# Kernel optimization log

Measured on AMD Instinct MI355X. Metric: run time of the kernel, lower is better.

## Reference

```python
import jax, jax.numpy as jnp
import numpy as np

B, CIN, COUT, H, W = 4, 256, 256, 64, 64
K, G = 3, 4
PAD = (K - 1) // 2


def setup_inputs() -> dict:
    key = jax.random.key(0)
    k0, k1, k2, k3 = jax.random.split(key, 4)
    x = jax.random.normal(k0, (B, CIN, H, W), jnp.float32)
    y = jax.random.normal(k1, (B, 2, H, W), jnp.float32)
    # conv_offset: 1x1 conv, no bias, init std=0.1 (normal_init)
    w_offset = jax.random.normal(k2, (G * 2 * K * K, 2, 1, 1), jnp.float32) * 0.1
    # DeformConv2d weight, no bias, init std=0.01
    w_deform = jax.random.normal(k3, (COUT, CIN, K, K), jnp.float32) * 0.01
    return {"x": x, "y": y, "w_offset": w_offset, "w_deform": w_deform}


def _deform_conv(x, offset, weight):
    """DCN v1: stride 1, dilation 1, zero padding PAD, deform_groups=G, groups=1."""
    KK = K * K
    # mmcv offset layout: [B, G*2*KK, H, W] -> per group, per kernel pos, (dy, dx)
    off = offset.reshape(B, G, KK, 2, H, W)
    dy, dx = off[:, :, :, 0], off[:, :, :, 1]            # [B,G,KK,H,W]
    ii, jj = jnp.meshgrid(jnp.arange(K), jnp.arange(K), indexing="ij")
    ky = ii.reshape(KK).astype(x.dtype)                  # kernel row offsets
    kx = jj.reshape(KK).astype(x.dtype)                  # kernel col offsets
    base_y = jnp.arange(H, dtype=x.dtype)[None, :, None] - PAD + ky[:, None, None]  # [KK,H,1]
    base_x = jnp.arange(W, dtype=x.dtype)[None, None, :] - PAD + kx[:, None, None]  # [KK,1,W]
    yc = dy + base_y                                     # [B,G,KK,H,W]
    xc = dx + base_x

    Cg = CIN // G
    xg = x.reshape(B, G, Cg, H, W)

    def sample(xg1, yc1, xc1):
        # xg1 [Cg,H,W]; yc1/xc1 [KK,H,W] -> bilinear sample with zero padding
        y0 = jnp.floor(yc1)
        x0 = jnp.floor(xc1)
        wy = yc1 - y0
        wx = xc1 - x0
        y0i = y0.astype(jnp.int32)
        x0i = x0.astype(jnp.int32)

        def gather(yi, xi):
            valid = (yi >= 0) & (yi < H) & (xi >= 0) & (xi < W)
            v = xg1[:, jnp.clip(yi, 0, H - 1), jnp.clip(xi, 0, W - 1)]  # [Cg,KK,H,W]
            return v * valid[None].astype(xg1.dtype)

        v00 = gather(y0i, x0i)
        v01 = gather(y0i, x0i + 1)
        v10 = gather(y0i + 1, x0i)
        v11 = gather(y0i + 1, x0i + 1)
        return (v00 * (1 - wy) * (1 - wx) + v01 * (1 - wy) * wx
                + v10 * wy * (1 - wx) + v11 * wy * wx)

    sampled = jax.vmap(jax.vmap(sample))(xg, yc, xc)     # [B,G,Cg,KK,H,W]
    sampled = sampled.reshape(B, CIN, KK, H, W)
    wflat = weight.reshape(COUT, CIN, KK)
    return jnp.einsum("bckhw,ock->bohw", sampled, wflat)  # [B,COUT,H,W]


def reference(x, y, w_offset, w_deform):
    # offset = conv_offset(y.detach()), a 1x1 conv without bias
    y_det = jax.lax.stop_gradient(y)
    offset = jnp.einsum("bihw,oi->bohw", y_det, w_offset[:, :, 0, 0])
    out = _deform_conv(x, offset, w_deform)
    return jax.nn.relu(out)
```

## Files before the change

### kernel.cpp

```cpp
#include <hip/hip_runtime.h>
#include <cstddef>

#define B_    4
#define CIN_  256
#define COUT_ 256
#define H_    64
#define W_    64
#define KK_   9
#define G_    4
#define NP    18
#define PW    80
#define PH    80
#define PADO  8

typedef short bf16x8 __attribute__((ext_vector_type(8)));
typedef float f32x4  __attribute__((ext_vector_type(4)));
typedef __attribute__((address_space(1))) const unsigned int* gptr_t;
typedef __attribute__((address_space(3))) unsigned int*       lptr_t;

__device__ __forceinline__ unsigned short f2bf(float v) {
    unsigned int u = __float_as_uint(v);
    u += 0x7fffu + ((u >> 16) & 1u);
    return (unsigned short)(u >> 16);
}
__device__ __forceinline__ float f_lo(unsigned int u) { return __uint_as_float(u << 16); }
__device__ __forceinline__ float f_hi(unsigned int u) { return __uint_as_float(u & 0xffff0000u); }

__global__ __launch_bounds__(256) void prep_kernel(const float* __restrict__ x,
                                                   unsigned short* __restrict__ xTp,
                                                   const float* __restrict__ w,
                                                   unsigned short* __restrict__ wb) {
    const int tid = threadIdx.x;
    if (blockIdx.x < 512) {
        __shared__ unsigned short s[128][66];
        const int bh    = blockIdx.x >> 1;
        const int chalf = blockIdx.x & 1;
        const int b     = bh >> 6, h = bh & 63;
        const size_t src_base = ((size_t)b * CIN_ + chalf * 128) * (H_ * W_) + h * W_;
        #pragma unroll 4
        for (int k = 0; k < 32; ++k) {
            int i = k * 256 + tid;
            int c = i >> 6, ww = i & 63;
            s[c][ww] = f2bf(x[src_base + (size_t)c * (H_ * W_) + ww]);
        }
        __syncthreads();
        const size_t dst_row = ((size_t)b * PH + (h + PADO)) * PW;
        #pragma unroll 4
        for (int k = 0; k < 20; ++k) {
            int j  = k * 256 + tid;
            int c2 = (j & 63) * 2, wp = j >> 6;
            unsigned int v = 0;
            if (wp >= PADO && wp < PADO + W_) {
                int ww = wp - PADO;
                v = (unsigned int)s[c2][ww] | ((unsigned int)s[c2 + 1][ww] << 16);
            }
            *(unsigned int*)(xTp + (dst_row + wp) * 256 + chalf * 128 + c2) = v;
        }
    } else if (blockIdx.x < 576) {
        const int bidx = blockIdx.x - 512;
        const int b = bidx >> 4, rr = bidx & 15;
        const int yp = (rr < PADO) ? rr : (PH - 16 + rr);
        unsigned short* dst = xTp + ((size_t)b * PH + yp) * PW * 256;
        #pragma unroll
        for (int k = 0; k < 10; ++k) {
            *(uint4*)(dst + (size_t)(k * 256 + tid) * 8) = make_uint4(0, 0, 0, 0);
        }
    } else {
        int idx = (blockIdx.x - 576) * 256 + tid;
        int e   = idx & 7;
        int pos = (idx >> 3) & 7;
        int o   = (idx >> 6) & 255;
        int t   = idx >> 14;
        int g   = t / 9, kk = t - g * 9;
        int j   = pos ^ (o & 7);
        int c   = g * 64 + j * 8 + e;
        wb[idx] = f2bf(w[(o * CIN_ + c) * KK_ + kk]);
    }
}

__global__ __launch_bounds__(512, 2) void dcn_kernel(
    const unsigned short* __restrict__ xTp, const float* __restrict__ y,
    const float* __restrict__ w_off, const unsigned short* __restrict__ wb,
    float* __restrict__ out)
{
    __shared__ unsigned short s_W[2][2][16384];
    __shared__ unsigned short s_S[2][2][4096];

    const int tid = threadIdx.x;
    const int bid = blockIdx.x;
    const int xcd = bid & 7;
    const int b   = xcd >> 1;
    const int h   = (xcd & 1) * 32 + (bid >> 3);

    const int sp = tid >> 3;
    const int c8 = tid & 7;

    const float yv0 = y[((b * 2 + 0) * H_ + h) * W_ + sp];
    const float yv1 = y[((b * 2 + 1) * H_ + h) * W_ + sp];
    const float spf = (float)(sp - 1 + PADO);
    const float hpf = (float)(h  - 1 + PADO);

    const int lane = tid & 63, wave = tid >> 6;
    const int pg  = wave & 1, oh = wave >> 1;
    const int l15 = lane & 15, kq = lane >> 4, sw = l15 & 7;

    f32x4 acc[8];
    #pragma unroll
    for (int i = 0; i < 8; ++i) acc[i] = (f32x4){0.f, 0.f, 0.f, 0.f};

    const unsigned short* xb = xTp + (size_t)b * (PH * PW * 256) + c8 * 8;

    float wgt[2][4];
    uint4 gA[2], gB[2], gC[2], gD[2];

#define ISSUE_ONE(t, P) do {                                                   \
    const int t_ = (t);                                                        \
    const int g_ = t_ / 9, kk_ = t_ - g_ * 9;                                  \
    const float4 co = *(const float4*)(w_off + t_ * 4);                        \
    const float dy = fmaf(yv0, co.x, yv1 * co.y);                              \
    const float dx = fmaf(yv0, co.z, yv1 * co.w);                              \
    const float yc = hpf + (float)(kk_ / 3) + dy;                              \
    const float xc = spf + (float)(kk_ % 3) + dx;                              \
    const float yf = floorf(yc), xf = floorf(xc);                              \
    const float wy = yc - yf, wx = xc - xf;                                    \
    const int   yi = (int)yf, xi = (int)xf;           \
    const float omy = 1.f - wy, omx = 1.f - wx;                                \
    wgt[P][0] = omy * omx; wgt[P][1] = omy * wx;                               \
    wgt[P][2] = wy * omx;  wgt[P][3] = wy * wx;                                \
    const unsigned short* p0 = xb + (yi * PW + xi) * 256 + g_ * 64;            \
    const unsigned short* p1 = p0 + PW * 256;                                  \
    gA[P] = *(const uint4*)(p0);        gB[P] = *(const uint4*)(p0 + 256);     \
    gC[P] = *(const uint4*)(p1);        gD[P] = *(const uint4*)(p1 + 256);     \
} while (0)

#define STAGE_W2(t, buf) do {                                                  \
    const unsigned short* src = wb + (size_t)(t) * 32768;                      \
    _Pragma("unroll")                                                          \
    for (int j = 0; j < 8; ++j) {                                              \
        const int off = (j * 512 + tid) * 8;                                   \
        __builtin_amdgcn_global_load_lds((gptr_t)(src + off),                  \
                                         (lptr_t)(&s_W[buf][0][0] + off),      \
                                         16, 0, 0);                            \
    }                                                                          \
} while (0)

#define WRITE_ONE(P, SB) do {                                                  \
    const unsigned int av[4] = {gA[P].x, gA[P].y, gA[P].z, gA[P].w};           \
    const unsigned int bv[4] = {gB[P].x, gB[P].y, gB[P].z, gB[P].w};           \
    const unsigned int cv[4] = {gC[P].x, gC[P].y, gC[P].z, gC[P].w};           \
    const unsigned int dv[4] = {gD[P].x, gD[P].y, gD[P].z, gD[P].w};           \
    unsigned int res[4];                                                       \
    _Pragma("unroll")                                                          \
    for (int q = 0; q < 4; ++q) {                                              \
        float rl = wgt[P][0] * f_lo(av[q]);                                    \
        rl = fmaf(wgt[P][1], f_lo(bv[q]), rl);                                 \
        rl = fmaf(wgt[P][2], f_lo(cv[q]), rl);                                 \
        rl = fmaf(wgt[P][3], f_lo(dv[q]), rl);                                 \
        float rh = wgt[P][0] * f_hi(av[q]);                                    \
        rh = fmaf(wgt[P][1], f_hi(bv[q]), rh);                                 \
        rh = fmaf(wgt[P][2], f_hi(cv[q]), rh);                                 \
        rh = fmaf(wgt[P][3], f_hi(dv[q]), rh);                                 \
        res[q] = __builtin_amdgcn_perm(__float_as_uint(rh),                    \
                                       __float_as_uint(rl), 0x07060302u);      \
    }                                                                          \
    *(uint4*)(&s_S[SB][P][0] + sp * 64 + ((c8 ^ (sp & 7)) * 8)) =              \
        make_uint4(res[0], res[1], res[2], res[3]);                            \
} while (0)

#define MFMA_TAP(WB, HF, SB) do {                                              \
    bf16x8 bf[2][2], af[2][4];                                                 \
    _Pragma("unroll")                                                          \
    for (int kh = 0; kh < 2; ++kh) {                                           \
        const int pos = ((kh * 4 + kq) ^ sw) * 8;                              \
        _Pragma("unroll")                                                      \
        for (int nt = 0; nt < 2; ++nt)                                         \
            bf[kh][nt] = *(const bf16x8*)(&s_S[SB][HF][0] +                    \
                              (pg * 32 + nt * 16 + l15) * 64 + pos);           \
        _Pragma("unroll")                                                      \
        for (int mt = 0; mt < 4; ++mt)                                         \
            af[kh][mt] = *(const bf16x8*)(&s_W[WB][HF][0] +                    \
                              (oh * 64 + mt * 16 + l15) * 64 + pos);           \
    }                                                                          \
    __builtin_amdgcn_s_setprio(1);                                             \
    _Pragma("unroll")                                                          \
    for (int kh = 0; kh < 2; ++kh)                                             \
        _Pragma("unroll")                                                      \
        for (int nt = 0; nt < 2; ++nt)                                         \
            _Pragma("unroll")                                                  \
            for (int mt = 0; mt < 4; ++mt)                                     \
                acc[nt * 4 + mt] = __builtin_amdgcn_mfma_f32_16x16x32_bf16(    \
                    af[kh][mt], bf[kh][nt], acc[nt * 4 + mt], 0, 0, 0);        \
    __builtin_amdgcn_s_setprio(0);                                             \
} while (0)

#define STEP(s_, P, DO_PF) do {                                                \
    if (DO_PF) { ISSUE_ONE(2 * (s_) + 2, 0); ISSUE_ONE(2 * (s_) + 3, 1); }     \
    __builtin_amdgcn_sched_barrier(0);                                         \
    if (DO_PF) STAGE_W2((s_) + 1, P ^ 1);                                      \
    __builtin_amdgcn_sched_barrier(0);                                         \
    MFMA_TAP(P, 0, P);                                                         \
    MFMA_TAP(P, 1, P);                                                         \
    __builtin_amdgcn_sched_barrier(0);                                         \
    if (DO_PF) { WRITE_ONE(0, P ^ 1); WRITE_ONE(1, P ^ 1); }                   \
    __builtin_amdgcn_sched_barrier(0);                                         \
    asm volatile("s_waitcnt vmcnt(0) lgkmcnt(0)" ::: "memory");                \
    __builtin_amdgcn_sched_barrier(0);                                         \
    __builtin_amdgcn_s_barrier();                                              \
    __builtin_amdgcn_sched_barrier(0);                                         \
} while (0)

    ISSUE_ONE(0, 0);
    ISSUE_ONE(1, 1);
    __builtin_amdgcn_sched_barrier(0);
    STAGE_W2(0, 0);
    __builtin_amdgcn_sched_barrier(0);
    WRITE_ONE(0, 0);
    WRITE_ONE(1, 0);
    __builtin_amdgcn_sched_barrier(0);
    asm volatile("s_waitcnt vmcnt(0) lgkmcnt(0)" ::: "memory");
    __builtin_amdgcn_sched_barrier(0);
    __builtin_amdgcn_s_barrier();
    __builtin_amdgcn_sched_barrier(0);

    for (int sb = 0; sb < 16; sb += 2) {
        STEP(sb + 0, 0, 1);
        STEP(sb + 1, 1, 1);
    }
    STEP(16, 0, 1);
    MFMA_TAP(1, 0, 1);
    MFMA_TAP(1, 1, 1);

    #pragma unroll
    for (int nt = 0; nt < 2; ++nt) {
        const int px = pg * 32 + nt * 16 + l15;
        #pragma unroll
        for (int mt = 0; mt < 4; ++mt) {
            const int obase = oh * 64 + mt * 16 + kq * 4;
            #pragma unroll
            for (int rr = 0; rr < 4; ++rr) {
                out[(((size_t)b * COUT_ + obase + rr) * H_ + h) * W_ + px] =
                    fmaxf(acc[nt * 4 + mt][rr], 0.f);
            }
        }
    }
#undef ISSUE_ONE
#undef STAGE_W2
#undef WRITE_ONE
#undef MFMA_TAP
#undef STEP
}

extern "C" void kernel_launch(void* const* d_in, const int* in_sizes, int n_in,
                              void* d_out, int out_size, void* d_ws, size_t ws_size,
                              hipStream_t stream) {
    const float* x     = (const float*)d_in[0];
    const float* y     = (const float*)d_in[1];
    const float* w_off = (const float*)d_in[2];
    const float* w_def = (const float*)d_in[3];
    float* out = (float*)d_out;

    unsigned short* xTp = (unsigned short*)d_ws;
    unsigned short* wb  = (unsigned short*)d_ws + (size_t)B_ * PH * PW * 256;

    prep_kernel<<<2880, 256, 0, stream>>>(x, xTp, w_def, wb);
    dcn_kernel<<<256, 512, 0, stream>>>(xTp, y, w_off, wb, out);
}
```

Before: 121.1 us.

## Warp-specialize DCN kernel into producer and MFMA consumer waves

Splits the 512-thread block so waves 4-7 only gather and bilinearly sample input and stage weight tiles into LDS, while waves 0-3 only run MFMAs, each covering 64 output channels and all 64 pixels. Weight staging moves to a triple buffer with one tap per stage, and sample staging to a double buffer, with partial vmcnt waits so global loads stay in flight across barriers. The intent is to overlap gather latency with matrix math instead of serializing them in every wave. In exchange each producer thread does twice the gather work, consumers hold 16 accumulators, and every tap now needs a block barrier.

```diff
diff --git a/kernel.cpp b/kernel.cpp
--- a/kernel.cpp
+++ b/kernel.cpp
@@ -8,7 +8,6 @@
 #define W_    64
 #define KK_   9
 #define G_    4
-#define NP    18
 #define PW    80
 #define PH    80
 #define PADO  8
@@ -83,37 +82,38 @@
     const float* __restrict__ w_off, const unsigned short* __restrict__ wb,
     float* __restrict__ out)
 {
-    __shared__ unsigned short s_W[2][2][16384];
-    __shared__ unsigned short s_S[2][2][4096];
+    __shared__ unsigned short s_W[3][16384];
+    __shared__ unsigned short s_S[2][4096];
 
     const int tid = threadIdx.x;
     const int bid = blockIdx.x;
     const int xcd = bid & 7;
     const int b   = xcd >> 1;
     const int h   = (xcd & 1) * 32 + (bid >> 3);
-
-    const int sp = tid >> 3;
-    const int c8 = tid & 7;
-
-    const float yv0 = y[((b * 2 + 0) * H_ + h) * W_ + sp];
-    const float yv1 = y[((b * 2 + 1) * H_ + h) * W_ + sp];
-    const float spf = (float)(sp - 1 + PADO);
-    const float hpf = (float)(h  - 1 + PADO);
-
     const int lane = tid & 63, wave = tid >> 6;
-    const int pg  = wave & 1, oh = wave >> 1;
-    const int l15 = lane & 15, kq = lane >> 4, sw = l15 & 7;
-
-    f32x4 acc[8];
-    #pragma unroll
-    for (int i = 0; i < 8; ++i) acc[i] = (f32x4){0.f, 0.f, 0.f, 0.f};
-
-    const unsigned short* xb = xTp + (size_t)b * (PH * PW * 256) + c8 * 8;
-
-    float wgt[2][4];
-    uint4 gA[2], gB[2], gC[2], gD[2];
-
-#define ISSUE_ONE(t, P) do {                                                   \
+
+#define BAR() do {                                                             \
+    __builtin_amdgcn_sched_barrier(0);                                         \
+    __builtin_amdgcn_s_barrier();                                              \
+    __builtin_amdgcn_sched_barrier(0);                                         \
+} while (0)
+
+    if (wave >= 4) {
+        const int ptid = tid - 256;
+        const int sp = ptid >> 2;
+        const int cq = (ptid & 3) * 2;
+
+        const float yv0 = y[((b * 2 + 0) * H_ + h) * W_ + sp];
+        const float yv1 = y[((b * 2 + 1) * H_ + h) * W_ + sp];
+        const float spf = (float)(sp - 1 + PADO);
+        const float hpf = (float)(h  - 1 + PADO);
+
+        const unsigned short* xb = xTp + (size_t)b * (PH * PW * 256) + cq * 8;
+
+        float wgt[2][4];
+        uint4 gA[2][2], gB[2][2], gC[2][2], gD[2][2];
+
+#define ISSUE_G(t, P) do {                                                     \
     const int t_ = (t);                                                        \
     const int g_ = t_ / 9, kk_ = t_ - g_ * 9;                                  \
     const float4 co = *(const float4*)(w_off + t_ * 4);                        \
@@ -129,27 +129,28 @@
     wgt[P][2] = wy * omx;  wgt[P][3] = wy * wx;                                \
     const unsigned short* p0 = xb + (yi * PW + xi) * 256 + g_ * 64;            \
     const unsigned short* p1 = p0 + PW * 256;                                  \
-    gA[P] = *(const uint4*)(p0);        gB[P] = *(const uint4*)(p0 + 256);     \
-    gC[P] = *(const uint4*)(p1);        gD[P] = *(const uint4*)(p1 + 256);     \
-} while (0)
-
-#define STAGE_W2(t, buf) do {                                                  \
-    const unsigned short* src = wb + (size_t)(t) * 32768;                      \
+    gA[P][0] = *(const uint4*)(p0);         gA[P][1] = *(const uint4*)(p0+8);  \
+    gB[P][0] = *(const uint4*)(p0 + 256);   gB[P][1] = *(const uint4*)(p0+264);\
+    gC[P][0] = *(const uint4*)(p1);         gC[P][1] = *(const uint4*)(p1+8);  \
+    gD[P][0] = *(const uint4*)(p1 + 256);   gD[P][1] = *(const uint4*)(p1+264);\
+} while (0)
+
+#define STAGE_W(t, buf) do {                                                   \
+    const unsigned short* src = wb + (size_t)(t) * 16384;                      \
     _Pragma("unroll")                                                          \
     for (int j = 0; j < 8; ++j) {                                              \
-        const int off = (j * 512 + tid) * 8;                                   \
+        const int off = (j * 256 + ptid) * 8;                                  \
         __builtin_amdgcn_global_load_lds((gptr_t)(src + off),                  \
-                                         (lptr_t)(&s_W[buf][0][0] + off),      \
+                                         (lptr_t)(&s_W[buf][0] + off),         \
                                          16, 0, 0);                            \
     }                                                                          \
 } while (0)
 
-#define WRITE_ONE(P, SB) do {                                                  \
-    const unsigned int av[4] = {gA[P].x, gA[P].y, gA[P].z, gA[P].w};           \
-    const unsigned int bv[4] = {gB[P].x, gB[P].y, gB[P].z, gB[P].w};           \
-    const unsigned int cv[4] = {gC[P].x, gC[P].y, gC[P].z, gC[P].w};           \
-    const unsigned int dv[4] = {gD[P].x, gD[P].y, gD[P].z, gD[P].w};           \
-    unsigned int res[4];                                                       \
+#define BIL1(Aq, Bq, Cq, Dq, P, res) do {                                      \
+    const unsigned int av[4] = {Aq.x, Aq.y, Aq.z, Aq.w};                       \
+    const unsigned int bv[4] = {Bq.x, Bq.y, Bq.z, Bq.w};                       \
+    const unsigned int cv[4] = {Cq.x, Cq.y, Cq.z, Cq.w};                       \
+    const unsigned int dv[4] = {Dq.x, Dq.y, Dq.z, Dq.w};                       \
     _Pragma("unroll")                                                          \
     for (int q = 0; q < 4; ++q) {                                              \
         float rl = wgt[P][0] * f_lo(av[q]);                                    \
@@ -163,91 +164,143 @@
         res[q] = __builtin_amdgcn_perm(__float_as_uint(rh),                    \
                                        __float_as_uint(rl), 0x07060302u);      \
     }                                                                          \
-    *(uint4*)(&s_S[SB][P][0] + sp * 64 + ((c8 ^ (sp & 7)) * 8)) =              \
-        make_uint4(res[0], res[1], res[2], res[3]);                            \
-} while (0)
-
-#define MFMA_TAP(WB, HF, SB) do {                                              \
-    bf16x8 bf[2][2], af[2][4];                                                 \
-    _Pragma("unroll")                                                          \
-    for (int kh = 0; kh < 2; ++kh) {                                           \
-        const int pos = ((kh * 4 + kq) ^ sw) * 8;                              \
-        _Pragma("unroll")                                                      \
-        for (int nt = 0; nt < 2; ++nt)                                         \
-            bf[kh][nt] = *(const bf16x8*)(&s_S[SB][HF][0] +                    \
-                              (pg * 32 + nt * 16 + l15) * 64 + pos);           \
+} while (0)
+
+#define BILIN2(P, SB) do {                                                     \
+    unsigned int r0[4], r1[4];                                                 \
+    BIL1(gA[P][0], gB[P][0], gC[P][0], gD[P][0], P, r0);                       \
+    BIL1(gA[P][1], gB[P][1], gC[P][1], gD[P][1], P, r1);                       \
+    *(uint4*)(&s_S[SB][0] + sp * 64 + (((cq + 0) ^ (sp & 7)) * 8)) =           \
+        make_uint4(r0[0], r0[1], r0[2], r0[3]);                                \
+    *(uint4*)(&s_S[SB][0] + sp * 64 + (((cq + 1) ^ (sp & 7)) * 8)) =           \
+        make_uint4(r1[0], r1[1], r1[2], r1[3]);                                \
+} while (0)
+
+#define PTAP(t, GSN, DBUF, GSO, SBUF) do {                                     \
+    ISSUE_G((t) + 2, GSN);                                                     \
+    __builtin_amdgcn_sched_barrier(0);                                         \
+    STAGE_W((t) + 2, DBUF);                                                    \
+    __builtin_amdgcn_sched_barrier(0);                                         \
+    asm volatile("s_waitcnt vmcnt(24)" ::: "memory");                          \
+    __builtin_amdgcn_sched_barrier(0);                                         \
+    BILIN2(GSO, SBUF);                                                         \
+    __builtin_amdgcn_sched_barrier(0);                                         \
+    asm volatile("s_waitcnt vmcnt(16) lgkmcnt(0)" ::: "memory");               \
+    BAR();                                                                     \
+} while (0)
+
+        ISSUE_G(0, 0);
+        __builtin_amdgcn_sched_barrier(0);
+        STAGE_W(0, 0);
+        __builtin_amdgcn_sched_barrier(0);
+        ISSUE_G(1, 1);
+        __builtin_amdgcn_sched_barrier(0);
+        STAGE_W(1, 1);
+        __builtin_amdgcn_sched_barrier(0);
+        asm volatile("s_waitcnt vmcnt(24)" ::: "memory");
+        __builtin_amdgcn_sched_barrier(0);
+        BILIN2(0, 0);
+        __builtin_amdgcn_sched_barrier(0);
+        asm volatile("s_waitcnt vmcnt(16) lgkmcnt(0)" ::: "memory");
+        BAR();
+
+        for (int tb = 0; tb < 30; tb += 6) {
+            PTAP(tb + 0, 0, 2, 1, 1);
+            PTAP(tb + 1, 1, 0, 0, 0);
+            PTAP(tb + 2, 0, 1, 1, 1);
+            PTAP(tb + 3, 1, 2, 0, 0);
+            PTAP(tb + 4, 0, 0, 1, 1);
+            PTAP(tb + 5, 1, 1, 0, 0);
+        }
+        PTAP(30, 0, 2, 1, 1);
+        PTAP(31, 1, 0, 0, 0);
+        PTAP(32, 0, 1, 1, 1);
+        PTAP(33, 1, 2, 0, 0);
+        asm volatile("s_waitcnt vmcnt(8)" ::: "memory");
+        __builtin_amdgcn_sched_barrier(0);
+        BILIN2(1, 1);
+        __builtin_amdgcn_sched_barrier(0);
+        asm volatile("s_waitcnt vmcnt(0) lgkmcnt(0)" ::: "memory");
+        BAR();
+        BAR();
+#undef ISSUE_G
+#undef STAGE_W
+#undef BIL1
+#undef BILIN2
+#undef PTAP
+    } else {
+        const int c   = wave;
+        const int l15 = lane & 15, kq = lane >> 4, swz = l15 & 7;
+        const int p0  = (kq ^ swz) * 8;
+        const int p1  = ((4 + kq) ^ swz) * 8;
+
+        const unsigned short* wbs[3] = {
+            &s_W[0][0] + (c * 64 + l15) * 64,
+            &s_W[1][0] + (c * 64 + l15) * 64,
+            &s_W[2][0] + (c * 64 + l15) * 64 };
+        const unsigned short* sbs[2] = {
+            &s_S[0][0] + l15 * 64,
+            &s_S[1][0] + l15 * 64 };
+
+        f32x4 acc[16];
+        #pragma unroll
+        for (int i = 0; i < 16; ++i) acc[i] = (f32x4){0.f, 0.f, 0.f, 0.f};
+
+#define CTAP(WB, SB) do {                                                      \
+    bf16x8 af0[4], af1[4], bf0[4], bf1[4];                                     \
+    _Pragma("unroll")                                                          \
+    for (int mt = 0; mt < 4; ++mt) {                                           \
+        af0[mt] = *(const bf16x8*)(wbs[WB] + mt * 1024 + p0);                  \
+        af1[mt] = *(const bf16x8*)(wbs[WB] + mt * 1024 + p1);                  \
+    }                                                                          \
+    _Pragma("unroll")                                                          \
+    for (int nt = 0; nt < 4; ++nt) {                                           \
+        bf0[nt] = *(const bf16x8*)(sbs[SB] + nt * 1024 + p0);                  \
+        bf1[nt] = *(const bf16x8*)(sbs[SB] + nt * 1024 + p1);                  \
+    }                                                                          \
+    __builtin_amdgcn_s_setprio(1);                                             \
+    _Pragma("unroll")                                                          \
+    for (int nt = 0; nt < 4; ++nt)                                             \
         _Pragma("unroll")                                                      \
         for (int mt = 0; mt < 4; ++mt)                                         \
-            af[kh][mt] = *(const bf16x8*)(&s_W[WB][HF][0] +                    \
-                              (oh * 64 + mt * 16 + l15) * 64 + pos);           \
-    }                                                                          \
-    __builtin_amdgcn_s_setprio(1);                                             \
-    _Pragma("unroll")                                                          \
-    for (int kh = 0; kh < 2; ++kh)                                             \
+            acc[nt * 4 + mt] = __builtin_amdgcn_mfma_f32_16x16x32_bf16(        \
+                af0[mt], bf0[nt], acc[nt * 4 + mt], 0, 0, 0);                  \
+    _Pragma("unroll")                                                          \
+    for (int nt = 0; nt < 4; ++nt)                                             \
         _Pragma("unroll")                                                      \
-        for (int nt = 0; nt < 2; ++nt)                                         \
-            _Pragma("unroll")                                                  \
-            for (int mt = 0; mt < 4; ++mt)                                     \
-                acc[nt * 4 + mt] = __builtin_amdgcn_mfma_f32_16x16x32_bf16(    \
-                    af[kh][mt], bf[kh][nt], acc[nt * 4 + mt], 0, 0, 0);        \
+        for (int mt = 0; mt < 4; ++mt)                                         \
+            acc[nt * 4 + mt] = __builtin_amdgcn_mfma_f32_16x16x32_bf16(        \
+                af1[mt], bf1[nt], acc[nt * 4 + mt], 0, 0, 0);                  \
     __builtin_amdgcn_s_setprio(0);                                             \
 } while (0)
 
-#define STEP(s_, P, DO_PF) do {                                                \
-    if (DO_PF) { ISSUE_ONE(2 * (s_) + 2, 0); ISSUE_ONE(2 * (s_) + 3, 1); }     \
-    __builtin_amdgcn_sched_barrier(0);                                         \
-    if (DO_PF) STAGE_W2((s_) + 1, P ^ 1);                                      \
-    __builtin_amdgcn_sched_barrier(0);                                         \
-    MFMA_TAP(P, 0, P);                                                         \
-    MFMA_TAP(P, 1, P);                                                         \
-    __builtin_amdgcn_sched_barrier(0);                                         \
-    if (DO_PF) { WRITE_ONE(0, P ^ 1); WRITE_ONE(1, P ^ 1); }                   \
-    __builtin_amdgcn_sched_barrier(0);                                         \
-    asm volatile("s_waitcnt vmcnt(0) lgkmcnt(0)" ::: "memory");                \
-    __builtin_amdgcn_sched_barrier(0);                                         \
-    __builtin_amdgcn_s_barrier();                                              \
-    __builtin_amdgcn_sched_barrier(0);                                         \
-} while (0)
-
-    ISSUE_ONE(0, 0);
-    ISSUE_ONE(1, 1);
-    __builtin_amdgcn_sched_barrier(0);
-    STAGE_W2(0, 0);
-    __builtin_amdgcn_sched_barrier(0);
-    WRITE_ONE(0, 0);
-    WRITE_ONE(1, 0);
-    __builtin_amdgcn_sched_barrier(0);
-    asm volatile("s_waitcnt vmcnt(0) lgkmcnt(0)" ::: "memory");
-    __builtin_amdgcn_sched_barrier(0);
-    __builtin_amdgcn_s_barrier();
-    __builtin_amdgcn_sched_barrier(0);
-
-    for (int sb = 0; sb < 16; sb += 2) {
-        STEP(sb + 0, 0, 1);
-        STEP(sb + 1, 1, 1);
+        BAR();
+        #pragma unroll 1
+        for (int g = 0; g < 6; ++g) {
+            CTAP(0, 0); BAR();
+            CTAP(1, 1); BAR();
+            CTAP(2, 0); BAR();
+            CTAP(0, 1); BAR();
+            CTAP(1, 0); BAR();
+            CTAP(2, 1); BAR();
+        }
+
+        #pragma unroll
+        for (int nt = 0; nt < 4; ++nt) {
+            const int px = nt * 16 + l15;
+            #pragma unroll
+            for (int mt = 0; mt < 4; ++mt) {
+                const int obase = c * 64 + mt * 16 + kq * 4;
+                #pragma unroll
+                for (int rr = 0; rr < 4; ++rr) {
+                    out[(((size_t)b * COUT_ + obase + rr) * H_ + h) * W_ + px] =
+                        fmaxf(acc[nt * 4 + mt][rr], 0.f);
+                }
+            }
+        }
+#undef CTAP
     }
-    STEP(16, 0, 1);
-    MFMA_TAP(1, 0, 1);
-    MFMA_TAP(1, 1, 1);
-
-    #pragma unroll
-    for (int nt = 0; nt < 2; ++nt) {
-        const int px = pg * 32 + nt * 16 + l15;
-        #pragma unroll
-        for (int mt = 0; mt < 4; ++mt) {
-            const int obase = oh * 64 + mt * 16 + kq * 4;
-            #pragma unroll
-            for (int rr = 0; rr < 4; ++rr) {
-                out[(((size_t)b * COUT_ + obase + rr) * H_ + h) * W_ + px] =
-                    fmaxf(acc[nt * 4 + mt][rr], 0.f);
-            }
-        }
-    }
-#undef ISSUE_ONE
-#undef STAGE_W2
-#undef WRITE_ONE
-#undef MFMA_TAP
-#undef STEP
+#undef BAR
 }
 
 extern "C" void kernel_launch(void* const* d_in, const int* in_sizes, int n_in,
```

New measurement: 120.5 us. About the same (-0.5%).

## Fuse prep and DCN kernels into one cooperative launch with grid sync

Applied to the files above, without the earlier changes.

The separate prep kernel (bf16 transpose/pad of x and weight repacking) is folded into the main DCN kernel, which now does the prep work itself and then waits on a cooperative-groups grid barrier. Each block transposes its own row of x through shared memory and writes part of the packed weights and the zero padding. This removes one kernel launch and the gap between the two kernels. In exchange it needs a cooperative launch and a grid-wide sync, and the prep now runs on only 256 blocks instead of 2880.

```diff
diff --git a/kernel.cpp b/kernel.cpp
--- a/kernel.cpp
+++ b/kernel.cpp
@@ -1,4 +1,5 @@
 #include <hip/hip_runtime.h>
+#include <hip/hip_cooperative_groups.h>
 #include <cstddef>
 
 #define B_    4
@@ -8,7 +9,6 @@
 #define W_    64
 #define KK_   9
 #define G_    4
-#define NP    18
 #define PW    80
 #define PH    80
 #define PADO  8
@@ -26,61 +26,10 @@
 __device__ __forceinline__ float f_lo(unsigned int u) { return __uint_as_float(u << 16); }
 __device__ __forceinline__ float f_hi(unsigned int u) { return __uint_as_float(u & 0xffff0000u); }
 
-__global__ __launch_bounds__(256) void prep_kernel(const float* __restrict__ x,
-                                                   unsigned short* __restrict__ xTp,
-                                                   const float* __restrict__ w,
-                                                   unsigned short* __restrict__ wb) {
-    const int tid = threadIdx.x;
-    if (blockIdx.x < 512) {
-        __shared__ unsigned short s[128][66];
-        const int bh    = blockIdx.x >> 1;
-        const int chalf = blockIdx.x & 1;
-        const int b     = bh >> 6, h = bh & 63;
-        const size_t src_base = ((size_t)b * CIN_ + chalf * 128) * (H_ * W_) + h * W_;
-        #pragma unroll 4
-        for (int k = 0; k < 32; ++k) {
-            int i = k * 256 + tid;
-            int c = i >> 6, ww = i & 63;
-            s[c][ww] = f2bf(x[src_base + (size_t)c * (H_ * W_) + ww]);
-        }
-        __syncthreads();
-        const size_t dst_row = ((size_t)b * PH + (h + PADO)) * PW;
-        #pragma unroll 4
-        for (int k = 0; k < 20; ++k) {
-            int j  = k * 256 + tid;
-            int c2 = (j & 63) * 2, wp = j >> 6;
-            unsigned int v = 0;
-            if (wp >= PADO && wp < PADO + W_) {
-                int ww = wp - PADO;
-                v = (unsigned int)s[c2][ww] | ((unsigned int)s[c2 + 1][ww] << 16);
-            }
-            *(unsigned int*)(xTp + (dst_row + wp) * 256 + chalf * 128 + c2) = v;
-        }
-    } else if (blockIdx.x < 576) {
-        const int bidx = blockIdx.x - 512;
-        const int b = bidx >> 4, rr = bidx & 15;
-        const int yp = (rr < PADO) ? rr : (PH - 16 + rr);
-        unsigned short* dst = xTp + ((size_t)b * PH + yp) * PW * 256;
-        #pragma unroll
-        for (int k = 0; k < 10; ++k) {
-            *(uint4*)(dst + (size_t)(k * 256 + tid) * 8) = make_uint4(0, 0, 0, 0);
-        }
-    } else {
-        int idx = (blockIdx.x - 576) * 256 + tid;
-        int e   = idx & 7;
-        int pos = (idx >> 3) & 7;
-        int o   = (idx >> 6) & 255;
-        int t   = idx >> 14;
-        int g   = t / 9, kk = t - g * 9;
-        int j   = pos ^ (o & 7);
-        int c   = g * 64 + j * 8 + e;
-        wb[idx] = f2bf(w[(o * CIN_ + c) * KK_ + kk]);
-    }
-}
-
-__global__ __launch_bounds__(512, 2) void dcn_kernel(
-    const unsigned short* __restrict__ xTp, const float* __restrict__ y,
-    const float* __restrict__ w_off, const unsigned short* __restrict__ wb,
+__global__ __launch_bounds__(512, 2) void dcn_fused(
+    const float* __restrict__ x, const float* __restrict__ y,
+    const float* __restrict__ w_off, const float* __restrict__ w_def,
+    unsigned short* __restrict__ xTp, unsigned short* __restrict__ wb,
     float* __restrict__ out)
 {
     __shared__ unsigned short s_W[2][2][16384];
@@ -91,6 +40,48 @@
     const int xcd = bid & 7;
     const int b   = xcd >> 1;
     const int h   = (xcd & 1) * 32 + (bid >> 3);
+
+    {
+        #pragma unroll
+        for (int r = 0; r < 5; ++r) {
+            int idx = r * 131072 + bid * 512 + tid;
+            if (idx < 589824) {
+                int e = idx & 7, pos = (idx >> 3) & 7, o = (idx >> 6) & 255;
+                int t = idx >> 14;
+                int g = t / 9, kk = t - g * 9;
+                int j = pos ^ (o & 7);
+                int c = g * 64 + j * 8 + e;
+                wb[idx] = f2bf(w_def[(o * 256 + c) * 9 + kk]);
+            }
+        }
+        if ((bid & 1) == 0 && (bid >> 3) < 16) {
+            int rr = bid >> 3;
+            int yp = rr < 8 ? rr : 64 + rr;
+            unsigned short* dz = xTp + ((size_t)b * PH + yp) * (PW * 256);
+            #pragma unroll
+            for (int k = 0; k < 5; ++k)
+                *(uint4*)(dz + (size_t)(k * 512 + tid) * 8) = make_uint4(0,0,0,0);
+        }
+        unsigned short* scr = &s_W[0][0][0];
+        #pragma unroll
+        for (int k = 0; k < 32; ++k) {
+            int i = k * 512 + tid; int c = i >> 6, w = i & 63;
+            scr[w * 264 + c] = f2bf(x[((size_t)(b * 256 + c) * 64 + h) * 64 + w]);
+        }
+        __syncthreads();
+        unsigned short* dr = xTp + ((size_t)b * PH + h + 8) * (PW * 256);
+        #pragma unroll
+        for (int k = 0; k < 5; ++k) {
+            int j = k * 512 + tid; int xp = j >> 5, ch = (j & 31) * 8;
+            uint4 v = make_uint4(0, 0, 0, 0);
+            if (xp >= 8 && xp < 72) v = *(const uint4*)(scr + (xp - 8) * 264 + ch);
+            *(uint4*)(dr + (size_t)xp * 256 + ch) = v;
+        }
+    }
+    __threadfence();
+    cooperative_groups::this_grid().sync();
+    __threadfence();
+    __syncthreads();
 
     const int sp = tid >> 3;
     const int c8 = tid & 7;
@@ -262,6 +253,8 @@
     unsigned short* xTp = (unsigned short*)d_ws;
     unsigned short* wb  = (unsigned short*)d_ws + (size_t)B_ * PH * PW * 256;
 
-    prep_kernel<<<2880, 256, 0, stream>>>(x, xTp, w_def, wb);
-    dcn_kernel<<<256, 512, 0, stream>>>(xTp, y, w_off, wb, out);
+    void* kargs[] = { (void*)&x, (void*)&y, (void*)&w_off, (void*)&w_def,
+                      (void*)&xTp, (void*)&wb, (void*)&out };
+    hipLaunchCooperativeKernel((const void*)dcn_fused, dim3(256), dim3(512),
+                               kargs, 0, stream);
 }
```

New measurement: 230.6 us. +90.5%, slower.
